# Optimization experiments

Measured on AMD Instinct MI355X. Metric: run time of the kernel, lower is better.

The kernel has to match this reference:

```python
import jax, jax.numpy as jnp
import numpy as np

HID = 2048
NUM_V, NUM_K = 32, 16
DK, DV = 128, 128
KEY_DIM = NUM_K * DK
VALUE_DIM = NUM_V * DV
CONV_DIM = 2 * KEY_DIM + VALUE_DIM
CONV_K = 4
CHUNK = 64
EPS = 1e-6
B, S = 2, 2048


def setup_inputs():
    key = jax.random.key(0)
    ks = jax.random.split(key, 9)
    w = lambda i, shape, sc=0.02: jax.random.normal(ks[i], shape, jnp.float32) * sc
    return {
        "hidden_states": jax.random.normal(ks[0], (B, S, HID), jnp.float32),
        "W_qkv": w(1, (HID, CONV_DIM)),
        "W_z": w(2, (HID, VALUE_DIM)),
        "W_b": w(3, (HID, NUM_V)),
        "W_a": w(4, (HID, NUM_V)),
        "conv_w": w(5, (CONV_DIM, CONV_K), 0.2),
        "dt_bias": jnp.ones((NUM_V,), jnp.float32),
        "A_log": jnp.log(jax.random.uniform(ks[6], (NUM_V,), jnp.float32, 1e-3, 16.0)),
        "norm_w": jnp.ones((DV,), jnp.float32),
        "W_out": w(7, (VALUE_DIM, HID)),
    }


def _l2norm(x, eps=1e-6):
    return x * jax.lax.rsqrt(jnp.sum(x * x, axis=-1, keepdims=True) + eps)


def _causal_conv_silu(x, w):
    # x: [B, C, S]; depthwise causal conv (kernel K), then SiLU. K is tiny (4).
    K = w.shape[-1]
    xp = jnp.pad(x, ((0, 0), (0, 0), (K - 1, 0)))
    out = sum(xp[:, :, j:j + x.shape[-1]] * w[None, :, j, None] for j in range(K))
    return jax.nn.silu(out)


def _chunk_gated_delta_rule(q, k, v, g, beta, chunk=CHUNK):
    # q,k: [B,S,H,DK]; v: [B,S,H,DV]; g,beta: [B,S,H]. S divisible by chunk.
    q, k = _l2norm(q), _l2norm(k)
    tr = lambda x: jnp.swapaxes(x, 1, 2)
    q, k, v, g, beta = tr(q), tr(k), tr(v), tr(g), tr(beta)  # [B,H,S,...]
    Bb, Hh, Ss, Dk = k.shape
    NC = Ss // chunk
    q = q * (Dk ** -0.5)
    k_beta = k * beta[..., None]
    v_beta = v * beta[..., None]
    ch = lambda x: x.reshape(Bb, Hh, NC, chunk, x.shape[-1])
    q, k, k_beta, v_beta = ch(q), ch(k), ch(k_beta), ch(v_beta)
    g = jnp.cumsum(g.reshape(Bb, Hh, NC, chunk), axis=-1)  # intra-chunk cumulative log-decay
    tril = jnp.tril(jnp.ones((chunk, chunk), bool))
    strict = jnp.tril(jnp.ones((chunk, chunk), bool), -1)
    diff = g[..., :, None] - g[..., None, :]
    dm = jnp.where(tril, jnp.exp(jnp.where(tril, diff, 0.0)), 0.0)  # decay mask, incl. diag
    # strictly-lower A; (I - A) is unit lower triangular -> M = (I - A)^{-1}
    A = -(k_beta @ jnp.swapaxes(k, -1, -2)) * dm * strict
    eye = jnp.eye(chunk, dtype=q.dtype)
    M = jax.scipy.linalg.solve_triangular(eye - A, jnp.broadcast_to(eye, A.shape), lower=True)
    v_c = M @ v_beta
    k_cd = M @ (k_beta * jnp.exp(g)[..., None])

    def step(state, xs):
        q_i, k_i, v_i, g_i, dm_i, kcd_i = xs
        attn_i = (q_i @ jnp.swapaxes(k_i, -1, -2)) * dm_i
        v_new = v_i - kcd_i @ state
        out = (q_i * jnp.exp(g_i)[..., None]) @ state + attn_i @ v_new
        g_last = g_i[..., -1:]
        k_dec = k_i * jnp.exp(g_last - g_i)[..., None]
        state = state * jnp.exp(g_last)[..., None] + jnp.einsum('bhck,bhcv->bhkv', k_dec, v_new)
        return state, out

    mv = lambda x: jnp.moveaxis(x, 2, 0)
    state0 = jnp.zeros((Bb, Hh, Dk, v_c.shape[-1]), q.dtype)
    _, outs = jax.lax.scan(step, state0, (mv(q), mv(k), mv(v_c), mv(g), mv(dm), mv(k_cd)))
    out = jnp.moveaxis(outs, 0, 2).reshape(Bb, Hh, Ss, -1)
    return jnp.swapaxes(out, 1, 2)  # [B,S,H,DV]


def reference(hidden_states, W_qkv, W_z, W_b, W_a, conv_w, dt_bias, A_log, norm_w, W_out):
    Bb, Ss, _ = hidden_states.shape
    mixed = jnp.swapaxes(hidden_states @ W_qkv, 1, 2)  # [B, CONV_DIM, S]
    z = (hidden_states @ W_z).reshape(Bb, Ss, NUM_V, DV)
    beta = jax.nn.sigmoid(hidden_states @ W_b)  # [B,S,NUM_V]
    g = -jnp.exp(A_log) * jax.nn.softplus((hidden_states @ W_a) + dt_bias)
    mixed = _causal_conv_silu(mixed, conv_w)
    mixed = jnp.swapaxes(mixed, 1, 2)  # [B,S,CONV_DIM]
    q = mixed[..., :KEY_DIM].reshape(Bb, Ss, NUM_K, DK)
    k = mixed[..., KEY_DIM:2 * KEY_DIM].reshape(Bb, Ss, NUM_K, DK)
    v = mixed[..., 2 * KEY_DIM:].reshape(Bb, Ss, NUM_V, DV)
    rep = NUM_V // NUM_K
    q = jnp.repeat(q, rep, axis=2)
    k = jnp.repeat(k, rep, axis=2)
    core = _chunk_gated_delta_rule(q, k, v, g, beta)  # [B,S,NUM_V,DV]
    # RMSNormGated: gate with silu(z) before normalization (Mamba2/Qwen3-Next style)
    gated = core * jax.nn.silu(z)
    var = jnp.mean(gated * gated, axis=-1, keepdims=True)
    core = gated * jax.lax.rsqrt(var + EPS) * norm_w
    return core.reshape(Bb, Ss, VALUE_DIM) @ W_out
```

## Files before the change

kernel.cpp:

```cpp
#include <hip/hip_runtime.h>
#include <cstdint>
#include <cstddef>


#define ROWS  4096
#define SEQ   2048
#define HIDN  2048
#define CONVD 8192
#define NWP   12544
#define NUMV  32

using bf16x8 = __attribute__((ext_vector_type(8))) short;
using f32x4v = __attribute__((ext_vector_type(4))) float;

__device__ __forceinline__ float bf2f(unsigned short u) {
  union { unsigned int i; float f; } x; x.i = ((unsigned int)u) << 16; return x.f;
}
__device__ __forceinline__ unsigned short f2bf(float f) {
  union { float f; unsigned int u; } x; x.f = f;
  unsigned int u = x.u;
  unsigned int r = (u + 0x7FFFu + ((u >> 16) & 1u)) >> 16;
  return (unsigned short)r;
}

typedef const __attribute__((address_space(1))) unsigned int GU32;
typedef __attribute__((address_space(3))) unsigned int LU32;
__device__ __forceinline__ void gld_lds16(const void* g, void* l) {
  GU32* gp = (GU32*)(unsigned long long)(uintptr_t)g;
  LU32* lp = (LU32*)(unsigned int)(uintptr_t)l;
  __builtin_amdgcn_global_load_lds(gp, lp, 16, 0, 0);
}
template <int N>
__device__ __forceinline__ void waitcnt_vm() {
  asm volatile("s_waitcnt vmcnt(%0)" ::"i"(N) : "memory");
}

__global__ __launch_bounds__(256) void cast_kernel(const float* __restrict__ in,
                                                   unsigned short* __restrict__ out, int n4) {
  int i = blockIdx.x * 256 + threadIdx.x;
  if (i >= n4) return;
  float4 v = ((const float4*)in)[i];
  ushort4 o;
  o.x = f2bf(v.x); o.y = f2bf(v.y); o.z = f2bf(v.z); o.w = f2bf(v.w);
  ((ushort4*)out)[i] = o;
}

__global__ __launch_bounds__(256) void transpose_kernel(const float* __restrict__ W,
                                                        unsigned short* __restrict__ WT,
                                                        int K, int N, int ld, int roff) {
  __shared__ float tile[64][65];
  const int t = threadIdx.x;
  const int kb = blockIdx.y * 64, nb = blockIdx.x * 64;
  const int r = t >> 2, c0 = (t & 3) * 16;
#pragma unroll
  for (int i = 0; i < 16; ++i) {
    int c = c0 + i;
    float v = 0.f;
    if (nb + c < N) v = W[(size_t)(kb + r) * N + nb + c];
    tile[r][c] = v;
  }
  __syncthreads();
  const int bn = t >> 2;
  if (nb + bn < N) {
#pragma unroll
    for (int i = 0; i < 16; ++i)
      WT[(size_t)(roff + nb + bn) * ld + kb + c0 + i] = f2bf(tile[c0 + i][bn]);
  }
}

template <int BM, int BN, int OUT_BF16>
__global__ __launch_bounds__(512) void gemm_ks_kernel(const unsigned short* __restrict__ Ag,
                                                      const unsigned short* __restrict__ Bg,
                                                      void* __restrict__ Cg, int M, int N, int K) {
  constexpr int PM = BM / 2, PN = BN / 4;
  constexpr int MT = PM / 16, NTF = PN / 16;
  constexpr int NA = BM / 128, NB = BN / 128;
  constexpr int LPS = NA + NB;
  constexpr int REG = (BM + BN) * 64;
  extern __shared__ char lds[];
  const int t = threadIdx.x;
  const int lane = t & 63, wid = t >> 6;
  const int wm = wid >> 2, wn = wid & 3;
  const int rlo = lane & 15, khi = lane >> 4;

  const int gx = gridDim.x, nwg = gx * gridDim.y;
  int id = blockIdx.y * gx + blockIdx.x;
  int sid = (id & 7) * (nwg >> 3) + (id >> 3);
  const int m0 = (sid / gx) * BM, n0 = (sid % gx) * BN;

  const int NT = K >> 6;
  const int NPH = NT * 2;

  const int srow = t >> 2;
  const int scs = ((t & 3) * 16) ^ (((t >> 3) & 3) << 4);
  const char* Ap[NA];
  const char* Bp[NB];
#pragma unroll
  for (int i = 0; i < NA; ++i)
    Ap[i] = (const char*)Ag + (size_t)(m0 + i * 128 + srow) * K * 2 + scs;
#pragma unroll
  for (int i = 0; i < NB; ++i)
    Bp[i] = (const char*)Bg + (size_t)(n0 + i * 128 + srow) * K * 2 + scs;
  char* dst = lds + t * 16;

  int offA[MT], offB[NTF];
#pragma unroll
  for (int mi = 0; mi < MT; ++mi) {
    int o = (wm * PM + mi * 16 + rlo) * 64 + khi * 16;
    o ^= ((o >> 7) & 3) << 4;
    offA[mi] = o;
  }
#pragma unroll
  for (int ni = 0; ni < NTF; ++ni) {
    int o = (wn * PN + ni * 16 + rlo) * 64 + khi * 16;
    o ^= ((o >> 7) & 3) << 4;
    offB[ni] = o + BM * 64;
  }

  f32x4v acc[MT][NTF];
#pragma unroll
  for (int mi = 0; mi < MT; ++mi)
#pragma unroll
    for (int ni = 0; ni < NTF; ++ni) acc[mi][ni] = (f32x4v){0.f, 0.f, 0.f, 0.f};

#define STG(PS)                                                              \
  do {                                                                       \
    int kts_ = ((PS) >> 1 < NT) ? ((PS) >> 1) : NT - 1;                      \
    size_t co_ = (size_t)kts_ * 128 + (size_t)((PS) & 1) * 64;               \
    char* d_ = dst + (((PS) & 3) * REG);                                     \
    _Pragma("unroll") for (int i_ = 0; i_ < NA; ++i_)                        \
        gld_lds16(Ap[i_] + co_, d_ + i_ * 8192);                             \
    _Pragma("unroll") for (int i_ = 0; i_ < NB; ++i_)                        \
        gld_lds16(Bp[i_] + co_, d_ + BM * 64 + i_ * 8192);                   \
  } while (0)

  STG(0); STG(1); STG(2);
  waitcnt_vm<2 * LPS>();
  __builtin_amdgcn_s_barrier();
  __builtin_amdgcn_sched_barrier(0);

#pragma unroll 1
  for (int p = 0; p < NPH; ++p) {
    const char* rb = lds + (p & 3) * REG;
    bf16x8 af[MT], bv[NTF];
#pragma unroll
    for (int mi = 0; mi < MT; ++mi) af[mi] = *(const bf16x8*)(rb + offA[mi]);
#pragma unroll
    for (int ni = 0; ni < NTF; ++ni) bv[ni] = *(const bf16x8*)(rb + offB[ni]);
    STG(p + 3);
    __builtin_amdgcn_s_setprio(1);
#pragma unroll
    for (int mi = 0; mi < MT; ++mi)
#pragma unroll
      for (int ni = 0; ni < NTF; ++ni)
        acc[mi][ni] = __builtin_amdgcn_mfma_f32_16x16x32_bf16(af[mi], bv[ni], acc[mi][ni], 0, 0, 0);
    __builtin_amdgcn_s_setprio(0);
    waitcnt_vm<2 * LPS>();
    __builtin_amdgcn_s_barrier();
    __builtin_amdgcn_sched_barrier(0);
  }
#undef STG
  waitcnt_vm<0>();

  const int mrb = khi * 4;
#pragma unroll
  for (int mi = 0; mi < MT; ++mi)
#pragma unroll
    for (int ni = 0; ni < NTF; ++ni)
#pragma unroll
      for (int r = 0; r < 4; ++r) {
        int mm = m0 + wm * PM + mi * 16 + mrb + r;
        int nn = n0 + wn * PN + ni * 16 + rlo;
        float v = acc[mi][ni][r];
        if (OUT_BF16) ((unsigned short*)Cg)[(size_t)mm * N + nn] = f2bf(v);
        else          ((float*)Cg)[(size_t)mm * N + nn] = v;
      }
}

__global__ __launch_bounds__(256) void conv_silu_kernel(const unsigned short* __restrict__ C1,
                                                        const float* __restrict__ conv_w,
                                                        unsigned short* __restrict__ QKV) {
  int idx = blockIdx.x * 256 + threadIdx.x;
  int row = idx >> 11;
  int c4 = (idx & 2047) << 2;
  int s = row & 2047;
  float4 w0 = *(const float4*)(conv_w + (size_t)(c4 + 0) * 4);
  float4 w1 = *(const float4*)(conv_w + (size_t)(c4 + 1) * 4);
  float4 w2 = *(const float4*)(conv_w + (size_t)(c4 + 2) * 4);
  float4 w3 = *(const float4*)(conv_w + (size_t)(c4 + 3) * 4);
  const float* pw0 = (const float*)&w0;
  const float* pw1 = (const float*)&w1;
  const float* pw2 = (const float*)&w2;
  const float* pw3 = (const float*)&w3;
  float a0 = 0.f, a1 = 0.f, a2 = 0.f, a3 = 0.f;
#pragma unroll
  for (int j = 0; j < 4; ++j) {
    int sr = s - 3 + j;
    if (sr < 0) continue;
    ushort4 mv = *(const ushort4*)(C1 + (size_t)(row - 3 + j) * NWP + c4);
    a0 += bf2f(mv.x) * pw0[j];
    a1 += bf2f(mv.y) * pw1[j];
    a2 += bf2f(mv.z) * pw2[j];
    a3 += bf2f(mv.w) * pw3[j];
  }
  ushort4 o;
  o.x = f2bf(a0 / (1.f + __expf(-a0)));
  o.y = f2bf(a1 / (1.f + __expf(-a1)));
  o.z = f2bf(a2 / (1.f + __expf(-a2)));
  o.w = f2bf(a3 / (1.f + __expf(-a3)));
  *(ushort4*)(QKV + (size_t)row * CONVD + c4) = o;
}

__global__ __launch_bounds__(256) void gbeta_kernel(const unsigned short* __restrict__ C1,
                                                    const float* __restrict__ dt_bias,
                                                    const float* __restrict__ A_log,
                                                    float* __restrict__ G, float* __restrict__ BETA) {
  int idx = blockIdx.x * 256 + threadIdx.x;
  int row = idx >> 5, h = idx & 31;
  float bp = bf2f(C1[(size_t)row * NWP + 12288 + h]);
  float ap = bf2f(C1[(size_t)row * NWP + 12320 + h]);
  BETA[idx] = 1.f / (1.f + __expf(-bp));
  float x = ap + dt_bias[h];
  float sp = (x > 15.f) ? x : log1pf(__expf(x));
  G[idx] = -__expf(A_log[h]) * sp;
}

#define INTRA_SMEM 70144
__global__ __launch_bounds__(256) void intra_kernel(const unsigned short* __restrict__ QKV,
                                                    const float* __restrict__ G,
                                                    const float* __restrict__ BETA,
                                                    unsigned short* __restrict__ WU,
                                                    unsigned short* __restrict__ ATTN) {
  extern __shared__ char smem[];
  unsigned short* ktb = (unsigned short*)smem;
  float* Amat = (float*)(smem + 17408);
  float* Xt   = (float*)(smem + 34816);
  unsigned short* qb = (unsigned short*)Xt;
  float* gc  = (float*)(smem + 69632);
  float* bet = gc + 64;

  const int t = threadIdx.x;
  const int lane = t & 63, w = t >> 6;
  const int rlo = lane & 15, khi = lane >> 4;
  const int cix = blockIdx.x & 31;
  const int h = (blockIdx.x >> 5) & 31;
  const int b = blockIdx.x >> 10;
  const int hq = h >> 1;
  const int row0 = cix * 64;
  const size_t rowbase = (size_t)b * SEQ;

  if (t < 64) {
    float gv = G[(rowbase + row0 + t) * NUMV + h];
    bet[t] = BETA[(rowbase + row0 + t) * NUMV + h];
#pragma unroll
    for (int off = 1; off < 64; off <<= 1) {
      float u = __shfl_up(gv, off, 64);
      if (t >= off) gv += u;
    }
    gc[t] = gv;
  }
  __syncthreads();

  const int r = t >> 2, q4 = t & 3;
  const size_t grow = (rowbase + row0 + r) * (size_t)CONVD;

  {
    const unsigned short* kp = QKV + grow + 2048 + hq * 128 + q4 * 32;
    float kv[32]; float ssk = 0.f;
#pragma unroll
    for (int j = 0; j < 32; j += 4) {
      ushort4 km = *(const ushort4*)(kp + j);
      kv[j] = bf2f(km.x); kv[j + 1] = bf2f(km.y); kv[j + 2] = bf2f(km.z); kv[j + 3] = bf2f(km.w);
      ssk += kv[j]*kv[j] + kv[j+1]*kv[j+1] + kv[j+2]*kv[j+2] + kv[j+3]*kv[j+3];
    }
    ssk += __shfl_xor(ssk, 1, 64);
    ssk += __shfl_xor(ssk, 2, 64);
    const float rk = rsqrtf(ssk + 1e-6f);
    const float ekr = __expf(gc[r]) * bet[r];
#pragma unroll
    for (int j = 0; j < 32; ++j) {
      float kn = kv[j] * rk;
      ktb[r * 136 + q4 * 32 + j] = f2bf(kn);
      Xt[(q4 * 32 + j) * 68 + r] = kn * ekr;
    }
  }
  __syncthreads();

  float xr[64];

  {
    static const signed char SJ[10][2] = {{0,0},{1,0},{1,1},{2,0},{2,1},{2,2},{3,0},{3,1},{3,2},{3,3}};
    static const signed char SB[5] = {0, 4, 7, 9, 10};
    for (int sj = SB[w]; sj < SB[w + 1]; ++sj) {
      const int mt = SJ[sj][0], nt = SJ[sj][1];
      f32x4v acc = (f32x4v){0.f, 0.f, 0.f, 0.f};
#pragma unroll
      for (int ks = 0; ks < 4; ++ks) {
        bf16x8 af = *(const bf16x8*)&ktb[(mt * 16 + rlo) * 136 + ks * 32 + khi * 8];
        bf16x8 bf_ = *(const bf16x8*)&ktb[(nt * 16 + rlo) * 136 + ks * 32 + khi * 8];
        acc = __builtin_amdgcn_mfma_f32_16x16x32_bf16(af, bf_, acc, 0, 0, 0);
      }
      const int j = nt * 16 + rlo;
#pragma unroll
      for (int r2 = 0; r2 < 4; ++r2) {
        const int i = mt * 16 + khi * 4 + r2;
        if (j < i) Amat[i * 68 + j] = -bet[i] * __expf(gc[i] - gc[j]) * acc[r2];
      }
    }
    if (t < 128) {
      const float* Xc = Xt + t * 68;
#pragma unroll
      for (int j = 0; j < 64; j += 4) {
        f32x4v xv = *(const f32x4v*)(Xc + j);
        xr[j] = xv[0]; xr[j + 1] = xv[1]; xr[j + 2] = xv[2]; xr[j + 3] = xv[3];
      }
    }
  }
  __syncthreads();

  {
    const unsigned short* vp = QKV + grow + 4096 + h * 128 + q4 * 32;
    const float brow = bet[r];
#pragma unroll
    for (int j = 0; j < 32; j += 4) {
      ushort4 vm = *(const ushort4*)(vp + j);
      Xt[(q4 * 32 + j + 0) * 68 + r] = bf2f(vm.x) * brow;
      Xt[(q4 * 32 + j + 1) * 68 + r] = bf2f(vm.y) * brow;
      Xt[(q4 * 32 + j + 2) * 68 + r] = bf2f(vm.z) * brow;
      Xt[(q4 * 32 + j + 3) * 68 + r] = bf2f(vm.w) * brow;
    }
  }
  __syncthreads();
  if (t >= 128) {
    const float* Xc = Xt + (t - 128) * 68;
#pragma unroll
    for (int j = 0; j < 64; j += 4) {
      f32x4v xv = *(const f32x4v*)(Xc + j);
      xr[j] = xv[0]; xr[j + 1] = xv[1]; xr[j + 2] = xv[2]; xr[j + 3] = xv[3];
    }
  }
  __syncthreads();

#pragma unroll
  for (int ib = 0; ib < 8; ++ib) {
    const int i0 = ib * 8;
    float p[8] = {0, 0, 0, 0, 0, 0, 0, 0};
#pragma unroll
    for (int j = 0; j < i0; j += 4) {
#pragma unroll
      for (int r2 = 0; r2 < 8; ++r2) {
        f32x4v ar = *(const f32x4v*)&Amat[(i0 + r2) * 68 + j];
        p[r2] += ar[0] * xr[j] + ar[1] * xr[j + 1] + ar[2] * xr[j + 2] + ar[3] * xr[j + 3];
      }
    }
#pragma unroll
    for (int r2 = 0; r2 < 8; ++r2) {
      float v = xr[i0 + r2] + p[r2];
#pragma unroll
      for (int r3 = 0; r3 < r2; ++r3) v += Amat[(i0 + r2) * 68 + i0 + r3] * xr[i0 + r3];
      xr[i0 + r2] = v;
    }
  }

  if (t < 128) {
    float* Xc = Xt + t * 68;
#pragma unroll
    for (int j = 0; j < 64; j += 4) {
      f32x4v xv = {xr[j], xr[j + 1], xr[j + 2], xr[j + 3]};
      *(f32x4v*)(Xc + j) = xv;
    }
  }
  __syncthreads();
  {
    unsigned short* wdst = WU + (rowbase + row0 + r) * (size_t)NWP + h * 128 + q4 * 32;
#pragma unroll
    for (int j = 0; j < 32; ++j) wdst[j] = f2bf(Xt[(q4 * 32 + j) * 68 + r]);
  }
  __syncthreads();
  if (t >= 128) {
    float* Xc = Xt + (t - 128) * 68;
#pragma unroll
    for (int j = 0; j < 64; j += 4) {
      f32x4v xv = {xr[j], xr[j + 1], xr[j + 2], xr[j + 3]};
      *(f32x4v*)(Xc + j) = xv;
    }
  }
  __syncthreads();
  {
    unsigned short* udst = WU + (rowbase + row0 + r) * (size_t)NWP + 4096 + h * 128 + q4 * 32;
#pragma unroll
    for (int j = 0; j < 32; ++j) udst[j] = f2bf(Xt[(q4 * 32 + j) * 68 + r]);
  }
  __syncthreads();

  {
    const unsigned short* qp = QKV + grow + hq * 128 + q4 * 32;
    float qv[32]; float ssq = 0.f;
#pragma unroll
    for (int j = 0; j < 32; j += 4) {
      ushort4 qm = *(const ushort4*)(qp + j);
      qv[j] = bf2f(qm.x); qv[j + 1] = bf2f(qm.y); qv[j + 2] = bf2f(qm.z); qv[j + 3] = bf2f(qm.w);
      ssq += qv[j]*qv[j] + qv[j+1]*qv[j+1] + qv[j+2]*qv[j+2] + qv[j+3]*qv[j+3];
    }
    ssq += __shfl_xor(ssq, 1, 64);
    ssq += __shfl_xor(ssq, 2, 64);
    const float rq = rsqrtf(ssq + 1e-6f) * 0.08838834764831845f;
#pragma unroll
    for (int j = 0; j < 32; ++j) qb[r * 136 + q4 * 32 + j] = f2bf(qv[j] * rq);
  }
  __syncthreads();

  {
    const size_t abase = (((size_t)b * 32 + h) * 32 + cix) * 4096;
#pragma unroll 1
    for (int nt = 0; nt < 4; ++nt) {
      const int j = nt * 16 + rlo;
      float vals[4] = {0.f, 0.f, 0.f, 0.f};
      if (nt <= w) {
        f32x4v acc = (f32x4v){0.f, 0.f, 0.f, 0.f};
#pragma unroll
        for (int ks = 0; ks < 4; ++ks) {
          bf16x8 af = *(const bf16x8*)&qb[(w * 16 + rlo) * 136 + ks * 32 + khi * 8];
          bf16x8 bf_ = *(const bf16x8*)&ktb[(nt * 16 + rlo) * 136 + ks * 32 + khi * 8];
          acc = __builtin_amdgcn_mfma_f32_16x16x32_bf16(af, bf_, acc, 0, 0, 0);
        }
#pragma unroll
        for (int r2 = 0; r2 < 4; ++r2) {
          const int i = w * 16 + khi * 4 + r2;
          if (j <= i) vals[r2] = __expf(gc[i] - gc[j]) * acc[r2];
        }
      }
#pragma unroll
      for (int r2 = 0; r2 < 4; ++r2)
        ATTN[abase + (w * 16 + khi * 4 + r2) * 64 + j] = f2bf(vals[r2]);
    }
  }
}

#define SEQ_SMEM 70400
__global__ __launch_bounds__(256) void seq_kernel(const unsigned short* __restrict__ QKV,
                                                  const float* __restrict__ G,
                                                  const unsigned short* __restrict__ WU,
                                                  const unsigned short* __restrict__ ATTN,
                                                  unsigned short* __restrict__ CORE) {
  extern __shared__ char smem[];
  unsigned short* ktT    = (unsigned short*)smem;
  unsigned short* wb     = (unsigned short*)(smem + 22528);
  unsigned short* attnb  = (unsigned short*)(smem + 39936);
  float* stateT          = (float*)(smem + 51200);
  unsigned short* stateTb = (unsigned short*)(smem + 59904);
  unsigned short* vnTb   = (unsigned short*)(smem + 64256);
  unsigned short* vdTb   = (unsigned short*)(smem + 67072);
  float* gc   = (float*)(smem + 69888);
  float* edec = (float*)(smem + 70144);

  const int t = threadIdx.x;
  const int lane = t & 63, w = t >> 6;
  const int rlo = lane & 15, khi = lane >> 4;
  const int vq = blockIdx.x & 7;
  const int h = (blockIdx.x >> 3) & 31;
  const int b = blockIdx.x >> 8;
  const int hq = h >> 1;
  const size_t rowbase = (size_t)b * SEQ;
  const size_t ahead = ((size_t)b * 32 + h) * 32;

  for (int i = t; i < 16 * 136; i += 256) { stateT[i] = 0.f; stateTb[i] = 0; }
  __syncthreads();

  bf16x8 qf[4];

#pragma unroll 1
  for (int ncb = 0; ncb < 32; ++ncb) {
    const int row0 = ncb * 64;

    if (t < 64) {
      float gv = G[(rowbase + row0 + t) * NUMV + h];
#pragma unroll
      for (int off = 1; off < 64; off <<= 1) {
        float u = __shfl_up(gv, off, 64);
        if (t >= off) gv += u;
      }
      gc[t] = gv;
      float tot = __shfl(gv, 63, 64);
      edec[t] = __expf(tot - gv);
    }
    __syncthreads();

    {
      const int r = t >> 2, q4 = t & 3;
      const size_t grow = (rowbase + row0 + r) * (size_t)CONVD;
      const unsigned short* kp = QKV + grow + 2048 + hq * 128 + q4 * 32;
      float kv[32]; float ssk = 0.f;
#pragma unroll
      for (int j = 0; j < 32; j += 4) {
        ushort4 km = *(const ushort4*)(kp + j);
        kv[j] = bf2f(km.x); kv[j + 1] = bf2f(km.y); kv[j + 2] = bf2f(km.z); kv[j + 3] = bf2f(km.w);
        ssk += kv[j]*kv[j] + kv[j+1]*kv[j+1] + kv[j+2]*kv[j+2] + kv[j+3]*kv[j+3];
      }
      ssk += __shfl_xor(ssk, 1, 64);
      ssk += __shfl_xor(ssk, 2, 64);
      const float rk = rsqrtf(ssk + 1e-6f);
#pragma unroll
      for (int j = 0; j < 32; ++j) ktT[(q4 * 32 + j) * 88 + r] = f2bf(kv[j] * rk);
      const unsigned short* wsrc = WU + (rowbase + row0 + r) * (size_t)NWP + h * 128 + q4 * 32;
#pragma unroll
      for (int u2 = 0; u2 < 4; ++u2)
        *(uint4*)&wb[r * 136 + q4 * 32 + u2 * 8] = *(const uint4*)(wsrc + u2 * 8);
      const unsigned short* asrc = ATTN + (ahead + ncb) * 4096 + r * 64 + q4 * 16;
      *(uint4*)&attnb[r * 88 + q4 * 16] = *(const uint4*)(asrc);
      *(uint4*)&attnb[r * 88 + q4 * 16 + 8] = *(const uint4*)(asrc + 8);
      const unsigned short* qsrc = QKV + (rowbase + row0 + w * 16 + rlo) * (size_t)CONVD + hq * 128 + khi * 8;
      float qv[32]; float ssq = 0.f;
#pragma unroll
      for (int ks = 0; ks < 4; ++ks) {
        ushort4 qa = *(const ushort4*)(qsrc + ks * 32);
        ushort4 qb2 = *(const ushort4*)(qsrc + ks * 32 + 4);
        qv[ks*8+0] = bf2f(qa.x); qv[ks*8+1] = bf2f(qa.y); qv[ks*8+2] = bf2f(qa.z); qv[ks*8+3] = bf2f(qa.w);
        qv[ks*8+4] = bf2f(qb2.x); qv[ks*8+5] = bf2f(qb2.y); qv[ks*8+6] = bf2f(qb2.z); qv[ks*8+7] = bf2f(qb2.w);
#pragma unroll
        for (int e = 0; e < 8; ++e) ssq += qv[ks*8+e] * qv[ks*8+e];
      }
      ssq += __shfl_xor(ssq, 16, 64);
      ssq += __shfl_xor(ssq, 32, 64);
      const float rq = rsqrtf(ssq + 1e-6f) * 0.08838834764831845f;
#pragma unroll
      for (int ks = 0; ks < 4; ++ks) {
        bf16x8 tv;
#pragma unroll
        for (int e = 0; e < 8; ++e) tv[e] = (short)f2bf(qv[ks*8+e] * rq);
        qf[ks] = tv;
      }
    }
    __syncthreads();

    f32x4v oacc;
    {
      f32x4v pacc = (f32x4v){0.f, 0.f, 0.f, 0.f};
      oacc = (f32x4v){0.f, 0.f, 0.f, 0.f};
#pragma unroll
      for (int ks = 0; ks < 4; ++ks) {
        bf16x8 aw = *(const bf16x8*)&wb[(w * 16 + rlo) * 136 + ks * 32 + khi * 8];
        bf16x8 bs = *(const bf16x8*)&stateTb[rlo * 136 + ks * 32 + khi * 8];
        pacc = __builtin_amdgcn_mfma_f32_16x16x32_bf16(aw, bs, pacc, 0, 0, 0);
        oacc = __builtin_amdgcn_mfma_f32_16x16x32_bf16(qf[ks], bs, oacc, 0, 0, 0);
      }
#pragma unroll
      for (int r2 = 0; r2 < 4; ++r2) {
        const int i = w * 16 + khi * 4 + r2;
        float uv = bf2f(WU[(rowbase + row0 + i) * (size_t)NWP + 4096 + h * 128 + vq * 16 + rlo]);
        float vn = uv - pacc[r2];
        vnTb[rlo * 88 + i] = f2bf(vn);
        vdTb[rlo * 88 + i] = f2bf(vn * edec[i]);
        oacc[r2] *= __expf(gc[i]);
      }
    }
    __syncthreads();

    {
#pragma unroll
      for (int ks = 0; ks < 2; ++ks) {
        bf16x8 aa = *(const bf16x8*)&attnb[(w * 16 + rlo) * 88 + ks * 32 + khi * 8];
        bf16x8 bv = *(const bf16x8*)&vnTb[rlo * 88 + ks * 32 + khi * 8];
        oacc = __builtin_amdgcn_mfma_f32_16x16x32_bf16(aa, bv, oacc, 0, 0, 0);
      }
      const int col = h * 128 + vq * 16 + rlo;
#pragma unroll
      for (int r2 = 0; r2 < 4; ++r2) {
        const int i = w * 16 + khi * 4 + r2;
        CORE[(rowbase + row0 + i) * (size_t)4096 + col] = f2bf(oacc[r2]);
      }
      const float egl = __expf(gc[63]);
#pragma unroll
      for (int n2 = 0; n2 < 2; ++n2) {
        const int dt = w * 2 + n2;
        f32x4v sacc = (f32x4v){0.f, 0.f, 0.f, 0.f};
#pragma unroll
        for (int ks = 0; ks < 2; ++ks) {
          bf16x8 ak = *(const bf16x8*)&ktT[(dt * 16 + rlo) * 88 + ks * 32 + khi * 8];
          bf16x8 bv2 = *(const bf16x8*)&vdTb[rlo * 88 + ks * 32 + khi * 8];
          sacc = __builtin_amdgcn_mfma_f32_16x16x32_bf16(ak, bv2, sacc, 0, 0, 0);
        }
#pragma unroll
        for (int r2 = 0; r2 < 4; ++r2) {
          const int d = dt * 16 + khi * 4 + r2;
          float ns = stateT[rlo * 136 + d] * egl + sacc[r2];
          stateT[rlo * 136 + d] = ns;
          stateTb[rlo * 136 + d] = f2bf(ns);
        }
      }
    }
    __syncthreads();
  }
}

__global__ __launch_bounds__(256) void gatenorm_kernel(const unsigned short* __restrict__ CORE,
                                                       const unsigned short* __restrict__ C1,
                                                       const float* __restrict__ norm_w,
                                                       unsigned short* __restrict__ NRM) {
  const int wid = blockIdx.x * 4 + (threadIdx.x >> 6);
  const int lane = threadIdx.x & 63;
  const int row = wid >> 5, h = wid & 31;
  const int c = lane * 2;
  const size_t cidx = (size_t)row * 4096 + h * 128 + c;
  const size_t zidx = (size_t)row * NWP + 8192 + h * 128 + c;
  float g0 = bf2f(CORE[cidx]), g1 = bf2f(CORE[cidx + 1]);
  float z0 = bf2f(C1[zidx]), z1 = bf2f(C1[zidx + 1]);
  g0 *= z0 / (1.f + __expf(-z0));
  g1 *= z1 / (1.f + __expf(-z1));
  float ss = g0 * g0 + g1 * g1;
#pragma unroll
  for (int m = 1; m < 64; m <<= 1) ss += __shfl_xor(ss, m, 64);
  const float rr = rsqrtf(ss * (1.f / 128.f) + 1e-6f);
  unsigned int o = ((unsigned int)f2bf(g1 * rr * norm_w[c + 1]) << 16) | (unsigned int)f2bf(g0 * rr * norm_w[c]);
  *(unsigned int*)(NRM + cidx) = o;
}

extern "C" void kernel_launch(void* const* d_in, const int* in_sizes, int n_in,
                              void* d_out, int out_size, void* d_ws, size_t ws_size,
                              hipStream_t stream) {
  const float* hs      = (const float*)d_in[0];
  const float* W_qkv   = (const float*)d_in[1];
  const float* W_z     = (const float*)d_in[2];
  const float* W_b     = (const float*)d_in[3];
  const float* W_a     = (const float*)d_in[4];
  const float* conv_w  = (const float*)d_in[5];
  const float* dt_bias = (const float*)d_in[6];
  const float* A_log   = (const float*)d_in[7];
  const float* norm_w  = (const float*)d_in[8];
  const float* W_out   = (const float*)d_in[9];
  float* out = (float*)d_out;
  char* ws = (char*)d_ws;

  const size_t OFF_HSB = 0;
  const size_t OFF_WT  = OFF_HSB + (size_t)ROWS * HIDN * 2;
  const size_t OFF_WOT = OFF_WT + (size_t)NWP * HIDN * 2;
  const size_t OFF_C1  = OFF_WOT + (size_t)HIDN * 4096 * 2;
  const size_t OFF_QKV = OFF_C1 + (size_t)ROWS * NWP * 2;
  const size_t OFF_G   = OFF_QKV + (size_t)ROWS * CONVD * 2;
  const size_t OFF_B   = OFF_G + (size_t)ROWS * NUMV * 4;

  unsigned short* hsb = (unsigned short*)(ws + OFF_HSB);
  unsigned short* WT  = (unsigned short*)(ws + OFF_WT);
  unsigned short* WoT = (unsigned short*)(ws + OFF_WOT);
  unsigned short* C1  = (unsigned short*)(ws + OFF_C1);
  unsigned short* QKV = (unsigned short*)(ws + OFF_QKV);
  float* Gb = (float*)(ws + OFF_G);
  float* Bb = (float*)(ws + OFF_B);
  unsigned short* ATTNb = (unsigned short*)(ws + OFF_HSB);
  unsigned short* COREb = (unsigned short*)(ws + OFF_WT);
  unsigned short* NRMb  = (unsigned short*)(ws + OFF_QKV);

  cast_kernel<<<ROWS * HIDN / 4 / 256, 256, 0, stream>>>(hs, hsb, ROWS * HIDN / 4);
  transpose_kernel<<<dim3(8192 / 64, 2048 / 64), 256, 0, stream>>>(W_qkv, WT, 2048, 8192, HIDN, 0);
  transpose_kernel<<<dim3(4096 / 64, 2048 / 64), 256, 0, stream>>>(W_z, WT, 2048, 4096, HIDN, 8192);
  transpose_kernel<<<dim3(1, 2048 / 64), 256, 0, stream>>>(W_b, WT, 2048, 32, HIDN, 12288);
  transpose_kernel<<<dim3(1, 2048 / 64), 256, 0, stream>>>(W_a, WT, 2048, 32, HIDN, 12320);
  hipMemsetAsync(ws + OFF_WT + (size_t)12352 * HIDN * 2, 0, (size_t)192 * HIDN * 2, stream);
  transpose_kernel<<<dim3(2048 / 64, 4096 / 64), 256, 0, stream>>>(W_out, WoT, 4096, 2048, 4096, 0);

  void (*g1p)(const unsigned short*, const unsigned short*, void*, int, int, int) = gemm_ks_kernel<256, 256, 1>;
  void (*g0p)(const unsigned short*, const unsigned short*, void*, int, int, int) = gemm_ks_kernel<128, 256, 0>;
  hipFuncSetAttribute((const void*)g1p, hipFuncAttributeMaxDynamicSharedMemorySize, 4 * (256 + 256) * 64);
  hipFuncSetAttribute((const void*)g0p, hipFuncAttributeMaxDynamicSharedMemorySize, 4 * (128 + 256) * 64);

  gemm_ks_kernel<256, 256, 1><<<dim3(NWP / 256, ROWS / 256), 512, 4 * (256 + 256) * 64, stream>>>(
      hsb, WT, C1, ROWS, NWP, HIDN);
  conv_silu_kernel<<<ROWS * (CONVD / 4) / 256, 256, 0, stream>>>(C1, conv_w, QKV);
  gbeta_kernel<<<ROWS * NUMV / 256, 256, 0, stream>>>(C1, dt_bias, A_log, Gb, Bb);

  hipFuncSetAttribute((const void*)intra_kernel, hipFuncAttributeMaxDynamicSharedMemorySize,
                      INTRA_SMEM);
  intra_kernel<<<2048, 256, INTRA_SMEM, stream>>>(QKV, Gb, Bb, C1, ATTNb);

  hipFuncSetAttribute((const void*)seq_kernel, hipFuncAttributeMaxDynamicSharedMemorySize,
                      SEQ_SMEM);
  seq_kernel<<<512, 256, SEQ_SMEM, stream>>>(QKV, Gb, C1, ATTNb, COREb);

  gatenorm_kernel<<<ROWS * NUMV / 4, 256, 0, stream>>>(COREb, C1, norm_w, NRMb);
  gemm_ks_kernel<128, 256, 0><<<dim3(2048 / 256, ROWS / 128), 512, 4 * (128 + 256) * 64, stream>>>(
      NRMb, WoT, out, ROWS, 2048, 4096);
}
```

Baseline: 815.3 us.

## Use 5-stage GEMM pipeline and rebalance several auxiliary kernels

The GEMM moves from a 4-slot LDS ring with a barrier every phase to a 5-slot ring that issues two phases per barrier. The goal is fewer synchronisations and more loads in flight, at the cost of more LDS, which may limit occupancy. Alongside this, the transpose writes are vectorised to 16-byte stores, and conv_silu computes 8 rows per thread so neighbouring input rows are reused. The intra kernel rebalances its triangular tile work across waves and has zero tiles written separately. The seq kernel keeps the cumulative decay in registers via shuffles, dropping an LDS round-trip and a barrier.

Measured after the change: 739.5 us. 9.3% less time.

```diff
diff --git a/kernel.cpp b/kernel.cpp
--- a/kernel.cpp
+++ b/kernel.cpp
@@ -60,16 +60,19 @@
     tile[r][c] = v;
   }
   __syncthreads();
-  const int bn = t >> 2;
+  const int bn = t >> 2, seg = (t & 3) * 16;
   if (nb + bn < N) {
-#pragma unroll
-    for (int i = 0; i < 16; ++i)
-      WT[(size_t)(roff + nb + bn) * ld + kb + c0 + i] = f2bf(tile[c0 + i][bn]);
+    unsigned short tmp[16];
+#pragma unroll
+    for (int i = 0; i < 16; ++i) tmp[i] = f2bf(tile[seg + i][bn]);
+    unsigned short* dst = WT + (size_t)(roff + nb + bn) * ld + kb + seg;
+    *(uint4*)dst = *(const uint4*)&tmp[0];
+    *(uint4*)(dst + 8) = *(const uint4*)&tmp[8];
   }
 }
 
 template <int BM, int BN, int OUT_BF16>
-__global__ __launch_bounds__(512) void gemm_ks_kernel(const unsigned short* __restrict__ Ag,
+__global__ __launch_bounds__(512) void gemm_r5_kernel(const unsigned short* __restrict__ Ag,
                                                       const unsigned short* __restrict__ Bg,
                                                       void* __restrict__ Cg, int M, int N, int K) {
   constexpr int PM = BM / 2, PN = BN / 4;
@@ -123,41 +126,66 @@
 #pragma unroll
     for (int ni = 0; ni < NTF; ++ni) acc[mi][ni] = (f32x4v){0.f, 0.f, 0.f, 0.f};
 
-#define STG(PS)                                                              \
+#define STG(PS, R)                                                           \
   do {                                                                       \
     int kts_ = ((PS) >> 1 < NT) ? ((PS) >> 1) : NT - 1;                      \
     size_t co_ = (size_t)kts_ * 128 + (size_t)((PS) & 1) * 64;               \
-    char* d_ = dst + (((PS) & 3) * REG);                                     \
+    char* d_ = dst + (size_t)(R) * REG;                                      \
     _Pragma("unroll") for (int i_ = 0; i_ < NA; ++i_)                        \
         gld_lds16(Ap[i_] + co_, d_ + i_ * 8192);                             \
     _Pragma("unroll") for (int i_ = 0; i_ < NB; ++i_)                        \
         gld_lds16(Bp[i_] + co_, d_ + BM * 64 + i_ * 8192);                   \
   } while (0)
 
-  STG(0); STG(1); STG(2);
-  waitcnt_vm<2 * LPS>();
+  STG(0, 0); STG(1, 1); STG(2, 2);
+  waitcnt_vm<LPS>();
   __builtin_amdgcn_s_barrier();
   __builtin_amdgcn_sched_barrier(0);
 
+  int rA = 0;
 #pragma unroll 1
-  for (int p = 0; p < NPH; ++p) {
-    const char* rb = lds + (p & 3) * REG;
-    bf16x8 af[MT], bv[NTF];
-#pragma unroll
-    for (int mi = 0; mi < MT; ++mi) af[mi] = *(const bf16x8*)(rb + offA[mi]);
-#pragma unroll
-    for (int ni = 0; ni < NTF; ++ni) bv[ni] = *(const bf16x8*)(rb + offB[ni]);
-    STG(p + 3);
-    __builtin_amdgcn_s_setprio(1);
-#pragma unroll
-    for (int mi = 0; mi < MT; ++mi)
-#pragma unroll
-      for (int ni = 0; ni < NTF; ++ni)
-        acc[mi][ni] = __builtin_amdgcn_mfma_f32_16x16x32_bf16(af[mi], bv[ni], acc[mi][ni], 0, 0, 0);
-    __builtin_amdgcn_s_setprio(0);
-    waitcnt_vm<2 * LPS>();
+  for (int q = 0; q < NPH / 2; ++q) {
+    const int p0 = q * 2;
+    int rB = rA + 1; if (rB >= 5) rB -= 5;
+    int tA = rA + 3; if (tA >= 5) tA -= 5;
+    int tB = rA + 4; if (tB >= 5) tB -= 5;
+
+    {
+      const char* rb = lds + (size_t)rA * REG;
+      bf16x8 af[MT], bv[NTF];
+#pragma unroll
+      for (int mi = 0; mi < MT; ++mi) af[mi] = *(const bf16x8*)(rb + offA[mi]);
+#pragma unroll
+      for (int ni = 0; ni < NTF; ++ni) bv[ni] = *(const bf16x8*)(rb + offB[ni]);
+      STG(p0 + 3, tA);
+      __builtin_amdgcn_s_setprio(1);
+#pragma unroll
+      for (int mi = 0; mi < MT; ++mi)
+#pragma unroll
+        for (int ni = 0; ni < NTF; ++ni)
+          acc[mi][ni] = __builtin_amdgcn_mfma_f32_16x16x32_bf16(af[mi], bv[ni], acc[mi][ni], 0, 0, 0);
+      __builtin_amdgcn_s_setprio(0);
+    }
+    {
+      const char* rb = lds + (size_t)rB * REG;
+      bf16x8 af[MT], bv[NTF];
+#pragma unroll
+      for (int mi = 0; mi < MT; ++mi) af[mi] = *(const bf16x8*)(rb + offA[mi]);
+#pragma unroll
+      for (int ni = 0; ni < NTF; ++ni) bv[ni] = *(const bf16x8*)(rb + offB[ni]);
+      STG(p0 + 4, tB);
+      __builtin_amdgcn_s_setprio(1);
+#pragma unroll
+      for (int mi = 0; mi < MT; ++mi)
+#pragma unroll
+        for (int ni = 0; ni < NTF; ++ni)
+          acc[mi][ni] = __builtin_amdgcn_mfma_f32_16x16x32_bf16(af[mi], bv[ni], acc[mi][ni], 0, 0, 0);
+      __builtin_amdgcn_s_setprio(0);
+    }
+    waitcnt_vm<LPS>();
     __builtin_amdgcn_s_barrier();
     __builtin_amdgcn_sched_barrier(0);
+    rA += 2; if (rA >= 5) rA -= 5;
   }
 #undef STG
   waitcnt_vm<0>();
@@ -181,9 +209,10 @@
                                                         const float* __restrict__ conv_w,
                                                         unsigned short* __restrict__ QKV) {
   int idx = blockIdx.x * 256 + threadIdx.x;
-  int row = idx >> 11;
+  int nb = idx >> 11;
   int c4 = (idx & 2047) << 2;
-  int s = row & 2047;
+  int row0 = nb * 8;
+  int s0 = row0 & 2047;
   float4 w0 = *(const float4*)(conv_w + (size_t)(c4 + 0) * 4);
   float4 w1 = *(const float4*)(conv_w + (size_t)(c4 + 1) * 4);
   float4 w2 = *(const float4*)(conv_w + (size_t)(c4 + 2) * 4);
@@ -192,23 +221,30 @@
   const float* pw1 = (const float*)&w1;
   const float* pw2 = (const float*)&w2;
   const float* pw3 = (const float*)&w3;
-  float a0 = 0.f, a1 = 0.f, a2 = 0.f, a3 = 0.f;
-#pragma unroll
-  for (int j = 0; j < 4; ++j) {
-    int sr = s - 3 + j;
-    if (sr < 0) continue;
-    ushort4 mv = *(const ushort4*)(C1 + (size_t)(row - 3 + j) * NWP + c4);
-    a0 += bf2f(mv.x) * pw0[j];
-    a1 += bf2f(mv.y) * pw1[j];
-    a2 += bf2f(mv.z) * pw2[j];
-    a3 += bf2f(mv.w) * pw3[j];
-  }
-  ushort4 o;
-  o.x = f2bf(a0 / (1.f + __expf(-a0)));
-  o.y = f2bf(a1 / (1.f + __expf(-a1)));
-  o.z = f2bf(a2 / (1.f + __expf(-a2)));
-  o.w = f2bf(a3 / (1.f + __expf(-a3)));
-  *(ushort4*)(QKV + (size_t)row * CONVD + c4) = o;
+  ushort4 rw[11];
+#pragma unroll
+  for (int i = 0; i < 11; ++i) {
+    if (s0 + i >= 3) rw[i] = *(const ushort4*)(C1 + (size_t)(row0 - 3 + i) * NWP + c4);
+    else { rw[i].x = 0; rw[i].y = 0; rw[i].z = 0; rw[i].w = 0; }
+  }
+#pragma unroll
+  for (int j = 0; j < 8; ++j) {
+    float a0 = 0.f, a1 = 0.f, a2 = 0.f, a3 = 0.f;
+#pragma unroll
+    for (int jj = 0; jj < 4; ++jj) {
+      ushort4 mv = rw[j + jj];
+      a0 += bf2f(mv.x) * pw0[jj];
+      a1 += bf2f(mv.y) * pw1[jj];
+      a2 += bf2f(mv.z) * pw2[jj];
+      a3 += bf2f(mv.w) * pw3[jj];
+    }
+    ushort4 o;
+    o.x = f2bf(a0 / (1.f + __expf(-a0)));
+    o.y = f2bf(a1 / (1.f + __expf(-a1)));
+    o.z = f2bf(a2 / (1.f + __expf(-a2)));
+    o.w = f2bf(a3 / (1.f + __expf(-a3)));
+    *(ushort4*)(QKV + (size_t)(row0 + j) * CONVD + c4) = o;
+  }
 }
 
 __global__ __launch_bounds__(256) void gbeta_kernel(const unsigned short* __restrict__ C1,
@@ -290,7 +326,7 @@
 
   {
     static const signed char SJ[10][2] = {{0,0},{1,0},{1,1},{2,0},{2,1},{2,2},{3,0},{3,1},{3,2},{3,3}};
-    static const signed char SB[5] = {0, 4, 7, 9, 10};
+    static const signed char SB[5] = {0, 3, 6, 8, 10};
     for (int sj = SB[w]; sj < SB[w + 1]; ++sj) {
       const int mt = SJ[sj][0], nt = SJ[sj][1];
       f32x4v acc = (f32x4v){0.f, 0.f, 0.f, 0.f};
@@ -412,27 +448,34 @@
 
   {
     const size_t abase = (((size_t)b * 32 + h) * 32 + cix) * 4096;
+    static const signed char CJ[10][2] = {{0,0},{1,0},{1,1},{2,0},{2,1},{2,2},{3,0},{3,1},{3,2},{3,3}};
+    static const signed char CB[5] = {0, 3, 6, 8, 10};
+    static const signed char ZJ[6][2] = {{0,1},{0,2},{0,3},{1,2},{1,3},{2,3}};
+    static const signed char ZB[5] = {0, 0, 0, 3, 6};
 #pragma unroll 1
-    for (int nt = 0; nt < 4; ++nt) {
+    for (int cj = CB[w]; cj < CB[w + 1]; ++cj) {
+      const int bi = CJ[cj][0], nt = CJ[cj][1];
       const int j = nt * 16 + rlo;
-      float vals[4] = {0.f, 0.f, 0.f, 0.f};
-      if (nt <= w) {
-        f32x4v acc = (f32x4v){0.f, 0.f, 0.f, 0.f};
-#pragma unroll
-        for (int ks = 0; ks < 4; ++ks) {
-          bf16x8 af = *(const bf16x8*)&qb[(w * 16 + rlo) * 136 + ks * 32 + khi * 8];
-          bf16x8 bf_ = *(const bf16x8*)&ktb[(nt * 16 + rlo) * 136 + ks * 32 + khi * 8];
-          acc = __builtin_amdgcn_mfma_f32_16x16x32_bf16(af, bf_, acc, 0, 0, 0);
-        }
-#pragma unroll
-        for (int r2 = 0; r2 < 4; ++r2) {
-          const int i = w * 16 + khi * 4 + r2;
-          if (j <= i) vals[r2] = __expf(gc[i] - gc[j]) * acc[r2];
-        }
-      }
+      f32x4v acc = (f32x4v){0.f, 0.f, 0.f, 0.f};
+#pragma unroll
+      for (int ks = 0; ks < 4; ++ks) {
+        bf16x8 af = *(const bf16x8*)&qb[(bi * 16 + rlo) * 136 + ks * 32 + khi * 8];
+        bf16x8 bf_ = *(const bf16x8*)&ktb[(nt * 16 + rlo) * 136 + ks * 32 + khi * 8];
+        acc = __builtin_amdgcn_mfma_f32_16x16x32_bf16(af, bf_, acc, 0, 0, 0);
+      }
+#pragma unroll
+      for (int r2 = 0; r2 < 4; ++r2) {
+        const int i = bi * 16 + khi * 4 + r2;
+        float v = (j <= i) ? __expf(gc[i] - gc[j]) * acc[r2] : 0.f;
+        ATTN[abase + i * 64 + j] = f2bf(v);
+      }
+    }
+#pragma unroll 1
+    for (int zj = ZB[w]; zj < ZB[w + 1]; ++zj) {
+      const int bi = ZJ[zj][0], nt = ZJ[zj][1];
 #pragma unroll
       for (int r2 = 0; r2 < 4; ++r2)
-        ATTN[abase + (w * 16 + khi * 4 + r2) * 64 + j] = f2bf(vals[r2]);
+        ATTN[abase + (bi * 16 + khi * 4 + r2) * 64 + nt * 16 + rlo] = 0;
     }
   }
 }
@@ -451,8 +494,6 @@
   unsigned short* stateTb = (unsigned short*)(smem + 59904);
   unsigned short* vnTb   = (unsigned short*)(smem + 64256);
   unsigned short* vdTb   = (unsigned short*)(smem + 67072);
-  float* gc   = (float*)(smem + 69888);
-  float* edec = (float*)(smem + 70144);
 
   const int t = threadIdx.x;
   const int lane = t & 63, w = t >> 6;
@@ -473,18 +514,13 @@
   for (int ncb = 0; ncb < 32; ++ncb) {
     const int row0 = ncb * 64;
 
-    if (t < 64) {
-      float gv = G[(rowbase + row0 + t) * NUMV + h];
-#pragma unroll
-      for (int off = 1; off < 64; off <<= 1) {
-        float u = __shfl_up(gv, off, 64);
-        if (t >= off) gv += u;
-      }
-      gc[t] = gv;
-      float tot = __shfl(gv, 63, 64);
-      edec[t] = __expf(tot - gv);
-    }
-    __syncthreads();
+    float gv = G[(rowbase + row0 + lane) * NUMV + h];
+#pragma unroll
+    for (int off = 1; off < 64; off <<= 1) {
+      float uph = __shfl_up(gv, off, 64);
+      if (lane >= off) gv += uph;
+    }
+    const float gtot = __shfl(gv, 63, 64);
 
     {
       const int r = t >> 2, q4 = t & 3;
@@ -547,11 +583,12 @@
 #pragma unroll
       for (int r2 = 0; r2 < 4; ++r2) {
         const int i = w * 16 + khi * 4 + r2;
+        const float gci = __shfl(gv, i, 64);
         float uv = bf2f(WU[(rowbase + row0 + i) * (size_t)NWP + 4096 + h * 128 + vq * 16 + rlo]);
         float vn = uv - pacc[r2];
         vnTb[rlo * 88 + i] = f2bf(vn);
-        vdTb[rlo * 88 + i] = f2bf(vn * edec[i]);
-        oacc[r2] *= __expf(gc[i]);
+        vdTb[rlo * 88 + i] = f2bf(vn * __expf(gtot - gci));
+        oacc[r2] *= __expf(gci);
       }
     }
     __syncthreads();
@@ -569,7 +606,7 @@
         const int i = w * 16 + khi * 4 + r2;
         CORE[(rowbase + row0 + i) * (size_t)4096 + col] = f2bf(oacc[r2]);
       }
-      const float egl = __expf(gc[63]);
+      const float egl = __expf(gtot);
 #pragma unroll
       for (int n2 = 0; n2 < 2; ++n2) {
         const int dt = w * 2 + n2;
@@ -658,14 +695,14 @@
   hipMemsetAsync(ws + OFF_WT + (size_t)12352 * HIDN * 2, 0, (size_t)192 * HIDN * 2, stream);
   transpose_kernel<<<dim3(2048 / 64, 4096 / 64), 256, 0, stream>>>(W_out, WoT, 4096, 2048, 4096, 0);
 
-  void (*g1p)(const unsigned short*, const unsigned short*, void*, int, int, int) = gemm_ks_kernel<256, 256, 1>;
-  void (*g0p)(const unsigned short*, const unsigned short*, void*, int, int, int) = gemm_ks_kernel<128, 256, 0>;
-  hipFuncSetAttribute((const void*)g1p, hipFuncAttributeMaxDynamicSharedMemorySize, 4 * (256 + 256) * 64);
-  hipFuncSetAttribute((const void*)g0p, hipFuncAttributeMaxDynamicSharedMemorySize, 4 * (128 + 256) * 64);
-
-  gemm_ks_kernel<256, 256, 1><<<dim3(NWP / 256, ROWS / 256), 512, 4 * (256 + 256) * 64, stream>>>(
+  void (*g1p)(const unsigned short*, const unsigned short*, void*, int, int, int) = gemm_r5_kernel<256, 256, 1>;
+  void (*g0p)(const unsigned short*, const unsigned short*, void*, int, int, int) = gemm_r5_kernel<128, 256, 0>;
+  hipFuncSetAttribute((const void*)g1p, hipFuncAttributeMaxDynamicSharedMemorySize, 5 * (256 + 256) * 64);
+  hipFuncSetAttribute((const void*)g0p, hipFuncAttributeMaxDynamicSharedMemorySize, 5 * (128 + 256) * 64);
+
+  gemm_r5_kernel<256, 256, 1><<<dim3(NWP / 256, ROWS / 256), 512, 5 * (256 + 256) * 64, stream>>>(
       hsb, WT, C1, ROWS, NWP, HIDN);
-  conv_silu_kernel<<<ROWS * (CONVD / 4) / 256, 256, 0, stream>>>(C1, conv_w, QKV);
+  conv_silu_kernel<<<(ROWS / 8) * 2048 / 256, 256, 0, stream>>>(C1, conv_w, QKV);
   gbeta_kernel<<<ROWS * NUMV / 256, 256, 0, stream>>>(C1, dt_bias, A_log, Gb, Bb);
 
   hipFuncSetAttribute((const void*)intra_kernel, hipFuncAttributeMaxDynamicSharedMemorySize,
@@ -677,6 +714,6 @@
   seq_kernel<<<512, 256, SEQ_SMEM, stream>>>(QKV, Gb, C1, ATTNb, COREb);
 
   gatenorm_kernel<<<ROWS * NUMV / 4, 256, 0, stream>>>(COREb, C1, norm_w, NRMb);
-  gemm_ks_kernel<128, 256, 0><<<dim3(2048 / 256, ROWS / 128), 512, 4 * (128 + 256) * 64, stream>>>(
+  gemm_r5_kernel<128, 256, 0><<<dim3(2048 / 256, ROWS / 128), 512, 5 * (128 + 256) * 64, stream>>>(
       NRMb, WoT, out, ROWS, 2048, 4096);
 }
```
